# Kernel optimization log

Hardware: AMD Instinct MI355X
Metric: run time of the kernel (lower is better)

The kernel has to match this reference:

```python
import jax, jax.numpy as jnp
import numpy as np

IN_FEATURES = 512
HIDDEN = 512


def setup_inputs() -> dict:
    key = jax.random.key(0)
    ks = jax.random.split(key, 7)
    s = 1.0 / np.sqrt(IN_FEATURES)
    return {
        "x": jax.random.normal(ks[0], (8, 2048, IN_FEATURES), dtype=jnp.float32),
        "Wq": jax.random.uniform(ks[1], (IN_FEATURES, HIDDEN), jnp.float32, -s, s),
        "bq": jax.random.uniform(ks[2], (HIDDEN,), jnp.float32, -s, s),
        "Wk": jax.random.uniform(ks[3], (IN_FEATURES, HIDDEN), jnp.float32, -s, s),
        "bk": jax.random.uniform(ks[4], (HIDDEN,), jnp.float32, -s, s),
        "Wv": jax.random.uniform(ks[5], (IN_FEATURES, HIDDEN), jnp.float32, -s, s),
        "bv": jax.random.uniform(ks[6], (HIDDEN,), jnp.float32, -s, s),
    }


def reference(x, Wq, bq, Wk, bk, Wv, bv):
    # q,k,v: [b, s, h]
    q = jnp.einsum("bsf,fh->bsh", x, Wq) + bq
    k = jnp.einsum("bsf,fh->bsh", x, Wk) + bk
    v = jnp.einsum("bsf,fh->bsh", x, Wv) + bv
    # NOTE: no 1/sqrt(d) scaling, matching the original module.
    scores = jnp.einsum("bqh,bkh->bqk", q, k)  # [b, s, s]
    attn = jax.nn.softmax(scores, axis=-1)
    return jnp.einsum("bqk,bkh->bqh", attn, v)
```

## Files before the change

### kernel.cpp

```cpp
#include <hip/hip_runtime.h>
#include <hip/hip_fp16.h>


typedef _Float16 f16;
typedef __attribute__((ext_vector_type(8))) _Float16 f16x8;
typedef __attribute__((ext_vector_type(4))) _Float16 f16x4;
typedef __attribute__((ext_vector_type(4))) float f32x4;
typedef __attribute__((address_space(3))) char lds_t;

#define GADDR(p) ((const __attribute__((address_space(1))) void*)(p))
#define LADDR(p) ((__attribute__((address_space(3))) void*)(p))

__device__ __forceinline__ unsigned lds_u32(void* p) {
    return (unsigned)(unsigned long long)(lds_t*)p;
}

#define DSRD(dst, a) asm volatile("ds_read_b128 %0, %1" : "=v"(dst) : "v"(a))
#define WAITV0 asm volatile("s_waitcnt vmcnt(0)" ::: "memory")
#define WAITV4 asm volatile("s_waitcnt vmcnt(4)" ::: "memory")
#define WAITV8 asm volatile("s_waitcnt vmcnt(8)" ::: "memory")
#define WAITLGKM0 asm volatile("s_waitcnt lgkmcnt(0)" ::: "memory")

__device__ __forceinline__ void xcd_remap(int& bx, int& by, int& bz) {
    const int gx = gridDim.x, gy = gridDim.y;
    const int nwg = gx * gy * gridDim.z;
    const int f = (blockIdx.z * gy + blockIdx.y) * gx + blockIdx.x;
    int L = (f & 7) * (nwg >> 3) + (f >> 3);
    bx = L % gx; int r = L / gx; by = r % gy; bz = r / gy;
}

__global__ __launch_bounds__(256) void k_cvt_x(const float* __restrict__ in,
                                               f16* __restrict__ out) {
    long i = (long)blockIdx.x * 256 + threadIdx.x;
    float4 v = ((const float4*)in)[i];
    f16x4 h = { (f16)v.x, (f16)v.y, (f16)v.z, (f16)v.w };
    ((f16x4*)out)[i] = h;
}

__global__ __launch_bounds__(256) void k_cvt_w(const float* __restrict__ Wq,
                                               const float* __restrict__ Wk,
                                               const float* __restrict__ Wv,
                                               f16* __restrict__ Wt) {
    int id = blockIdx.x * 256 + threadIdx.x;
    int w = id >> 18, rem = id & 262143;
    int kk = rem >> 9, n = rem & 511;
    const float* W = (w == 0) ? Wq : (w == 1) ? Wk : Wv;
    Wt[((long)w << 18) + ((long)n << 9) + kk] = (f16)W[((long)kk << 9) + n];
}

__global__ __launch_bounds__(256) void k_transpose_v(const f16* __restrict__ V,
                                                     f16* __restrict__ Vt) {
    __shared__ f16 t[32][33];
    int b = blockIdx.z, s0 = blockIdx.y * 32, d0 = blockIdx.x * 32;
    int x = threadIdx.x & 31, y = threadIdx.x >> 5;
#pragma unroll
    for (int i = 0; i < 4; ++i)
        t[y + i * 8][x] = V[((long)(b * 2048 + s0 + y + i * 8) << 9) + d0 + x];
    __syncthreads();
#pragma unroll
    for (int i = 0; i < 4; ++i)
        Vt[((long)(b * 512 + d0 + y + i * 8) << 11) + s0 + x] = t[x][y + i * 8];
}


#define STAGE8(HBASE, SRC, LD, ROWB, K0)                                                        \
  { const f16* s0_ = (SRC) + ((ROWB) + (tid >> 3)) * (long)(LD) + (K0) + colSw;                 \
    __builtin_amdgcn_global_load_lds(GADDR(s0_), LADDR(smem + (HBASE) + wid * 1024), 16, 0, 0); \
    const f16* s1_ = (SRC) + ((ROWB) + 64 + (tid >> 3)) * (long)(LD) + (K0) + colSw;            \
    __builtin_amdgcn_global_load_lds(GADDR(s1_), LADDR(smem + (HBASE) + 8192 + wid * 1024), 16, 0, 0); }

#define PHASE8(BUF, MH, NH, STAGE_CODE, WAIT_CODE)                                   \
  {                                                                                  \
    f16x8 af[4][2], bf[2][2];                                                        \
    const unsigned aB = sbase + (BUF) * 65536u + (MH) * 16384u;                      \
    const unsigned bB = sbase + (BUF) * 65536u + 32768u + (NH) * 16384u;             \
    _Pragma("unroll") for (int mi = 0; mi < 4; ++mi) {                               \
      unsigned ra = wm2 * 64 + mi * 16 + l15;                                        \
      DSRD(af[mi][0], aB + ra * 128 + cb0);                                          \
      DSRD(af[mi][1], aB + ra * 128 + cb1);                                          \
    }                                                                                \
    _Pragma("unroll") for (int nj = 0; nj < 2; ++nj) {                               \
      unsigned rb = wn2 * 32 + nj * 16 + l15;                                        \
      DSRD(bf[nj][0], bB + rb * 128 + cb0);                                          \
      DSRD(bf[nj][1], bB + rb * 128 + cb1);                                          \
    }                                                                                \
    STAGE_CODE;                                                                      \
    WAIT_CODE;                                                                       \
    __builtin_amdgcn_s_barrier();                                                    \
    WAITLGKM0;                                                                       \
    __builtin_amdgcn_sched_barrier(0);                                               \
    __builtin_amdgcn_s_setprio(1);                                                   \
    _Pragma("unroll") for (int mi = 0; mi < 4; ++mi)                                 \
      _Pragma("unroll") for (int nj = 0; nj < 2; ++nj)                               \
        _Pragma("unroll") for (int ks = 0; ks < 2; ++ks)                             \
          acc[MH][NH][mi][nj] = __builtin_amdgcn_mfma_f32_16x16x32_f16(              \
              af[mi][ks], bf[nj][ks], acc[MH][NH][mi][nj], 0, 0, 0);                 \
    __builtin_amdgcn_s_setprio(0);                                                   \
    __builtin_amdgcn_s_barrier();                                                    \
  }

template <bool OUT_F16, bool QKV>
__global__ __launch_bounds__(512) void k_gemm8(const f16* __restrict__ A,
                                               const f16* __restrict__ Bt,
                                               void* __restrict__ Cv,
                                               void* __restrict__ CvAlt,
                                               const float* __restrict__ b0,
                                               const float* __restrict__ b1,
                                               const float* __restrict__ b2,
                                               int M, int N, int K,
                                               long sA, long sB, long sC) {
    int bxi, byi, bz;
    xcd_remap(bxi, byi, bz);
    A  += bz * sA;
    Bt += bz * sB;
    __shared__ __align__(16) char smem[131072];
    const unsigned sbase = lds_u32(smem);

    const int tid = threadIdx.x;
    const int wid = tid >> 6, lane = tid & 63;
    const int l15 = lane & 15, l4 = lane >> 4;
    const int wm2 = wid >> 2, wn2 = wid & 3;
    const long rowA0 = (long)byi * 256;
    const long rowB0 = (long)bxi * 256;

    const unsigned sw = (unsigned)((l15 & 7) << 4);
    const unsigned cb0 = (unsigned)(l4 * 16) ^ sw;
    const unsigned cb1 = (unsigned)(64 + l4 * 16) ^ sw;
    const int colSw = (((tid & 7) ^ ((tid >> 3) & 7)) << 3);

    f32x4 acc[2][2][4][2] = {};

    const int NT = K >> 6;

    STAGE8(0,             A,  K, rowA0,       0);
    STAGE8(32768,         Bt, K, rowB0,       0);
    STAGE8(16384,         A,  K, rowA0 + 128, 0);
    STAGE8(32768 + 16384, Bt, K, rowB0 + 128, 0);
    STAGE8(65536,         A,  K, rowA0,       64);
    STAGE8(65536 + 32768, Bt, K, rowB0,       64);
    WAITV4;
    __builtin_amdgcn_s_barrier();

    for (int t = 0; t < NT; t += 2) {
        const bool more = (t + 2 < NT);
        const int k1 = (t + 1) << 6, k2 = (t + 2) << 6, k3 = (t + 3) << 6;
        PHASE8(0, 0, 0, { STAGE8(65536 + 16384,         A,  K, rowA0 + 128, k1); }, );
        PHASE8(0, 0, 1, { STAGE8(65536 + 32768 + 16384, Bt, K, rowB0 + 128, k1); }, );
        PHASE8(0, 1, 0, { if (more) STAGE8(0,             A,  K, rowA0,       k2); }, );
        PHASE8(0, 1, 1, { if (more) STAGE8(32768,         Bt, K, rowB0,       k2); },
                        { if (more) WAITV4; else WAITV0; });
        PHASE8(1, 0, 0, { if (more) STAGE8(16384,         A,  K, rowA0 + 128, k2); }, );
        PHASE8(1, 0, 1, { if (more) STAGE8(32768 + 16384, Bt, K, rowB0 + 128, k2); }, );
        PHASE8(1, 1, 0, { if (more) STAGE8(65536,         A,  K, rowA0,       k3); }, );
        PHASE8(1, 1, 1, { if (more) STAGE8(65536 + 32768, Bt, K, rowB0,       k3); },
                        { if (more) WAITV4; else WAITV0; });
    }

    const float* bias = nullptr;
    if constexpr (QKV) bias = (bz == 0) ? b0 : (bz == 1) ? b1 : b2;

#pragma unroll
    for (int MH = 0; MH < 2; ++MH)
#pragma unroll
        for (int NH = 0; NH < 2; ++NH)
#pragma unroll
            for (int mi = 0; mi < 4; ++mi)
#pragma unroll
                for (int nj = 0; nj < 2; ++nj) {
                    long gr = rowA0 + MH * 128 + wm2 * 64 + mi * 16 + l4 * 4;
                    int  gc = (int)rowB0 + NH * 128 + wn2 * 32 + nj * 16 + l15;
                    float bv_ = QKV ? bias[gc] : 0.f;
                    if constexpr (OUT_F16) {
                        f16* C;
                        if constexpr (QKV) C = (bz < 2) ? (f16*)Cv + bz * sC : (f16*)CvAlt;
                        else               C = (f16*)Cv + bz * sC;
#pragma unroll
                        for (int r = 0; r < 4; ++r)
                            C[(gr + r) * (long)N + gc] = (f16)(acc[MH][NH][mi][nj][r] + bv_);
                    } else {
                        float* C = (float*)Cv + bz * sC;
#pragma unroll
                        for (int r = 0; r < 4; ++r)
                            C[(gr + r) * (long)N + gc] = acc[MH][NH][mi][nj][r] + bv_;
                    }
                }
}

#define PVSTAGE(BUF, K0)                                                                    \
  { _Pragma("unroll") for (int i_ = 0; i_ < 4; ++i_) {                                      \
      const f16* sa_ = A + (rowA0 + i_ * 32 + (tid >> 3)) * (long)K + (K0) + colSw;         \
      __builtin_amdgcn_global_load_lds(GADDR(sa_),                                          \
          LADDR(smem + (BUF) * 32768 + i_ * 4096 + wave * 1024), 16, 0, 0);                 \
      const f16* sb_ = Bt + (rowB0 + i_ * 32 + (tid >> 3)) * (long)K + (K0) + colSw;        \
      __builtin_amdgcn_global_load_lds(GADDR(sb_),                                          \
          LADDR(smem + (BUF) * 32768 + 16384 + i_ * 4096 + wave * 1024), 16, 0, 0);         \
    } }

__global__ __launch_bounds__(256) void k_pv(const f16* __restrict__ Ain,
                                            const f16* __restrict__ Btin,
                                            float* __restrict__ Cout,
                                            int N, int K,
                                            long sA, long sB, long sC) {
    int bxi, byi, bz;
    xcd_remap(bxi, byi, bz);
    const f16* A  = Ain  + bz * sA;
    const f16* Bt = Btin + bz * sB;
    __shared__ __align__(16) char smem[65536];
    const unsigned sbase = lds_u32(smem);

    const int tid = threadIdx.x;
    const int wave = tid >> 6, lane = tid & 63;
    const int l15 = lane & 15, l4 = lane >> 4;
    const int wm = (wave >> 1) * 64, wn = (wave & 1) * 64;
    const long rowA0 = (long)byi * 128;
    const long rowB0 = (long)bxi * 128;

    const unsigned sw = (unsigned)((l15 & 7) << 4);
    const unsigned cb0 = (unsigned)(l4 * 16) ^ sw;
    const unsigned cb1 = (unsigned)(64 + l4 * 16) ^ sw;
    const int colSw = (((tid & 7) ^ ((tid >> 3) & 7)) << 3);

    f32x4 acc[4][4] = {};

    const int nt = K >> 6;
    PVSTAGE(0, 0);
    int cur = 0;
    for (int t = 0; t < nt; ++t) {
        if (t + 1 < nt) { PVSTAGE(cur ^ 1, (t + 1) << 6); WAITV8; }
        else            { WAITV0; }
        __builtin_amdgcn_s_barrier();

        f16x8 af[4][2], bf[4][2];
        const unsigned aB = sbase + (unsigned)cur * 32768u;
        const unsigned bB = aB + 16384u;
#pragma unroll
        for (int mi = 0; mi < 4; ++mi) {
            unsigned ra = wm + mi * 16 + l15;
            DSRD(af[mi][0], aB + ra * 128 + cb0);
            DSRD(af[mi][1], aB + ra * 128 + cb1);
        }
#pragma unroll
        for (int nj = 0; nj < 4; ++nj) {
            unsigned rb = wn + nj * 16 + l15;
            DSRD(bf[nj][0], bB + rb * 128 + cb0);
            DSRD(bf[nj][1], bB + rb * 128 + cb1);
        }
        WAITLGKM0;
        __builtin_amdgcn_sched_barrier(0);
        __builtin_amdgcn_s_setprio(1);
#pragma unroll
        for (int mi = 0; mi < 4; ++mi)
#pragma unroll
            for (int nj = 0; nj < 4; ++nj)
#pragma unroll
                for (int ks = 0; ks < 2; ++ks)
                    acc[mi][nj] = __builtin_amdgcn_mfma_f32_16x16x32_f16(
                        af[mi][ks], bf[nj][ks], acc[mi][nj], 0, 0, 0);
        __builtin_amdgcn_s_setprio(0);
        __builtin_amdgcn_s_barrier();
        cur ^= 1;
    }

    float* C = Cout + bz * sC;
#pragma unroll
    for (int mi = 0; mi < 4; ++mi)
#pragma unroll
        for (int nj = 0; nj < 4; ++nj) {
            long gr = rowA0 + wm + mi * 16 + l4 * 4;
            int  gc = (int)rowB0 + wn + nj * 16 + l15;
#pragma unroll
            for (int r = 0; r < 4; ++r)
                C[(gr + r) * (long)N + gc] = acc[mi][nj][r];
        }
}

__global__ __launch_bounds__(256) void k_softmax(f16* __restrict__ P) {
    const long row = blockIdx.x;
    f16* p = P + row * 2048;
    const int tid = threadIdx.x, lane = tid & 63, wave = tid >> 6;

    f16x8 v = ((const f16x8*)p)[tid];
    float f[8];
#pragma unroll
    for (int j = 0; j < 8; ++j) f[j] = (float)v[j];
    float m = fmaxf(fmaxf(fmaxf(f[0], f[1]), fmaxf(f[2], f[3])),
                    fmaxf(fmaxf(f[4], f[5]), fmaxf(f[6], f[7])));
#pragma unroll
    for (int off = 32; off; off >>= 1) m = fmaxf(m, __shfl_xor(m, off));

    __shared__ float red[4];
    __shared__ float bc[2];
    if (lane == 0) red[wave] = m;
    __syncthreads();
    if (tid == 0) bc[0] = fmaxf(fmaxf(red[0], red[1]), fmaxf(red[2], red[3]));
    __syncthreads();
    m = bc[0];

    float e[8], sum = 0.f;
#pragma unroll
    for (int j = 0; j < 8; ++j) { e[j] = __expf(f[j] - m); sum += e[j]; }
#pragma unroll
    for (int off = 32; off; off >>= 1) sum += __shfl_xor(sum, off);
    if (lane == 0) red[wave] = sum;
    __syncthreads();
    if (tid == 0) bc[1] = (red[0] + red[1]) + (red[2] + red[3]);
    __syncthreads();
    float inv = 1.f / bc[1];

    f16x8 o;
#pragma unroll
    for (int j = 0; j < 8; ++j) o[j] = (f16)(e[j] * inv);
    ((f16x8*)p)[tid] = o;
}

extern "C" void kernel_launch(void* const* d_in, const int* in_sizes, int n_in,
                              void* d_out, int out_size, void* d_ws, size_t ws_size,
                              hipStream_t stream) {
    const float* x  = (const float*)d_in[0];
    const float* Wq = (const float*)d_in[1];
    const float* bq = (const float*)d_in[2];
    const float* Wk = (const float*)d_in[3];
    const float* bk = (const float*)d_in[4];
    const float* Wv = (const float*)d_in[5];
    const float* bv = (const float*)d_in[6];
    float* out = (float*)d_out;

    char* ws = (char*)d_ws;
    f16* qh = (f16*)(ws + 0);
    f16* kh = (f16*)(ws + 16777216);
    f16* P8 = (f16*)(ws + 33554432);
    f16* Wt = (f16*)(ws + 33554432);
    f16* vt = (f16*)(ws + 0);
    f16* xh = (f16*)d_out;
    f16* vv = (f16*)((char*)d_out + 16777216);

    k_cvt_x<<<8192, 256, 0, stream>>>(x, xh);
    k_cvt_w<<<3072, 256, 0, stream>>>(Wq, Wk, Wv, Wt);

    k_gemm8<true, true><<<dim3(2, 64, 3), 512, 0, stream>>>(
        xh, Wt, qh, vv, bq, bk, bv, 16384, 512, 512,
        0, (long)512 * 512, (long)16384 * 512);

    k_gemm8<true, false><<<dim3(8, 8, 8), 512, 0, stream>>>(
        qh, kh, P8, nullptr, nullptr, nullptr, nullptr, 2048, 2048, 512,
        (long)2048 * 512, (long)2048 * 512, (long)2048 * 2048);

    k_transpose_v<<<dim3(16, 64, 8), 256, 0, stream>>>(vv, vt);

    k_softmax<<<16384, 256, 0, stream>>>(P8);

    k_pv<<<dim3(4, 16, 8), 256, 0, stream>>>(
        P8, vt, out, 512, 2048,
        (long)2048 * 2048, (long)512 * 2048, (long)2048 * 512);
}
```

Measured before the change: 174.4 us.

## Software-pipeline LDS fragment loads across MFMA phases with double-buffered A fragments

Restructures the GEMM inner loop from eight phases of 16 MFMAs into four phases of 32 MFMAs. B fragments for both N halves load once per K-tile, and A fragments are double-buffered in registers so the next phase's LDS reads run during the current phase's MFMAs. Partial lgkmcnt waits replace full drains, and the number of barriers per K-tile pair drops. This adds register pressure from the extra fragment sets and relies on careful ordering of the LDS waits.

New measurement: 299.2 us. 1.72x slower.

```diff
diff --git a/kernel.cpp b/kernel.cpp
--- a/kernel.cpp
+++ b/kernel.cpp
@@ -19,7 +19,7 @@
 #define WAITV0 asm volatile("s_waitcnt vmcnt(0)" ::: "memory")
 #define WAITV4 asm volatile("s_waitcnt vmcnt(4)" ::: "memory")
 #define WAITV8 asm volatile("s_waitcnt vmcnt(8)" ::: "memory")
-#define WAITLGKM0 asm volatile("s_waitcnt lgkmcnt(0)" ::: "memory")
+#define WAITLG(n) asm volatile("s_waitcnt lgkmcnt(" #n ")" ::: "memory")
 
 __device__ __forceinline__ void xcd_remap(int& bx, int& by, int& bz) {
     const int gx = gridDim.x, gy = gridDim.y;
@@ -69,35 +69,32 @@
     const f16* s1_ = (SRC) + ((ROWB) + 64 + (tid >> 3)) * (long)(LD) + (K0) + colSw;            \
     __builtin_amdgcn_global_load_lds(GADDR(s1_), LADDR(smem + (HBASE) + 8192 + wid * 1024), 16, 0, 0); }
 
-#define PHASE8(BUF, MH, NH, STAGE_CODE, WAIT_CODE)                                   \
-  {                                                                                  \
-    f16x8 af[4][2], bf[2][2];                                                        \
-    const unsigned aB = sbase + (BUF) * 65536u + (MH) * 16384u;                      \
-    const unsigned bB = sbase + (BUF) * 65536u + 32768u + (NH) * 16384u;             \
-    _Pragma("unroll") for (int mi = 0; mi < 4; ++mi) {                               \
-      unsigned ra = wm2 * 64 + mi * 16 + l15;                                        \
-      DSRD(af[mi][0], aB + ra * 128 + cb0);                                          \
-      DSRD(af[mi][1], aB + ra * 128 + cb1);                                          \
-    }                                                                                \
+#define LOAD_AF(AFSET, BUF, MH)                                                      \
+  _Pragma("unroll") for (int mi = 0; mi < 4; ++mi) {                                 \
+    unsigned ra = wm2 * 64 + mi * 16 + l15;                                          \
+    DSRD(AFSET[mi][0], sbase + (BUF) * 65536u + (MH) * 16384u + ra * 128 + cb0);     \
+    DSRD(AFSET[mi][1], sbase + (BUF) * 65536u + (MH) * 16384u + ra * 128 + cb1);     \
+  }
+
+#define LOAD_BF(BUF)                                                                 \
+  _Pragma("unroll") for (int nh = 0; nh < 2; ++nh)                                   \
     _Pragma("unroll") for (int nj = 0; nj < 2; ++nj) {                               \
       unsigned rb = wn2 * 32 + nj * 16 + l15;                                        \
-      DSRD(bf[nj][0], bB + rb * 128 + cb0);                                          \
-      DSRD(bf[nj][1], bB + rb * 128 + cb1);                                          \
-    }                                                                                \
-    STAGE_CODE;                                                                      \
-    WAIT_CODE;                                                                       \
-    __builtin_amdgcn_s_barrier();                                                    \
-    WAITLGKM0;                                                                       \
-    __builtin_amdgcn_sched_barrier(0);                                               \
-    __builtin_amdgcn_s_setprio(1);                                                   \
-    _Pragma("unroll") for (int mi = 0; mi < 4; ++mi)                                 \
+      DSRD(bf[nh][nj][0], sbase + (BUF) * 65536u + 32768u + nh * 16384u + rb * 128 + cb0); \
+      DSRD(bf[nh][nj][1], sbase + (BUF) * 65536u + 32768u + nh * 16384u + rb * 128 + cb1); \
+    }
+
+#define MFMA_Q(MH, AFSET)                                                            \
+  __builtin_amdgcn_sched_barrier(0);                                                 \
+  __builtin_amdgcn_s_setprio(1);                                                     \
+  _Pragma("unroll") for (int mi = 0; mi < 4; ++mi)                                   \
+    _Pragma("unroll") for (int nh = 0; nh < 2; ++nh)                                 \
       _Pragma("unroll") for (int nj = 0; nj < 2; ++nj)                               \
         _Pragma("unroll") for (int ks = 0; ks < 2; ++ks)                             \
-          acc[MH][NH][mi][nj] = __builtin_amdgcn_mfma_f32_16x16x32_f16(              \
-              af[mi][ks], bf[nj][ks], acc[MH][NH][mi][nj], 0, 0, 0);                 \
-    __builtin_amdgcn_s_setprio(0);                                                   \
-    __builtin_amdgcn_s_barrier();                                                    \
-  }
+          acc[MH][nh][mi][nj] = __builtin_amdgcn_mfma_f32_16x16x32_f16(              \
+              AFSET[mi][ks], bf[nh][nj][ks], acc[MH][nh][mi][nj], 0, 0, 0);          \
+  __builtin_amdgcn_s_setprio(0);                                                     \
+  __builtin_amdgcn_s_barrier();
 
 template <bool OUT_F16, bool QKV>
 __global__ __launch_bounds__(512) void k_gemm8(const f16* __restrict__ A,
@@ -128,6 +125,7 @@
     const unsigned cb1 = (unsigned)(64 + l4 * 16) ^ sw;
     const int colSw = (((tid & 7) ^ ((tid >> 3) & 7)) << 3);
 
+    f16x8 afA[4][2], afB[4][2], bf[2][2][2];
     f32x4 acc[2][2][4][2] = {};
 
     const int NT = K >> 6;
@@ -140,20 +138,46 @@
     STAGE8(65536 + 32768, Bt, K, rowB0,       64);
     WAITV4;
     __builtin_amdgcn_s_barrier();
+    LOAD_AF(afA, 0, 0);
 
     for (int t = 0; t < NT; t += 2) {
         const bool more = (t + 2 < NT);
         const int k1 = (t + 1) << 6, k2 = (t + 2) << 6, k3 = (t + 3) << 6;
-        PHASE8(0, 0, 0, { STAGE8(65536 + 16384,         A,  K, rowA0 + 128, k1); }, );
-        PHASE8(0, 0, 1, { STAGE8(65536 + 32768 + 16384, Bt, K, rowB0 + 128, k1); }, );
-        PHASE8(0, 1, 0, { if (more) STAGE8(0,             A,  K, rowA0,       k2); }, );
-        PHASE8(0, 1, 1, { if (more) STAGE8(32768,         Bt, K, rowB0,       k2); },
-                        { if (more) WAITV4; else WAITV0; });
-        PHASE8(1, 0, 0, { if (more) STAGE8(16384,         A,  K, rowA0 + 128, k2); }, );
-        PHASE8(1, 0, 1, { if (more) STAGE8(32768 + 16384, Bt, K, rowB0 + 128, k2); }, );
-        PHASE8(1, 1, 0, { if (more) STAGE8(65536,         A,  K, rowA0,       k3); }, );
-        PHASE8(1, 1, 1, { if (more) STAGE8(65536 + 32768, Bt, K, rowB0,       k3); },
-                        { if (more) WAITV4; else WAITV0; });
+
+        STAGE8(65536 + 16384,         A,  K, rowA0 + 128, k1);
+        STAGE8(65536 + 32768 + 16384, Bt, K, rowB0 + 128, k1);
+        __builtin_amdgcn_s_barrier();
+        LOAD_BF(0);
+        LOAD_AF(afB, 0, 1);
+        WAITLG(8);
+        MFMA_Q(0, afA);
+
+        if (more) { STAGE8(0,     A,  K, rowA0, k2);
+                    STAGE8(32768, Bt, K, rowB0, k2);
+                    WAITV4; }
+        else      { WAITV0; }
+        __builtin_amdgcn_s_barrier();
+        LOAD_AF(afA, 1, 0);
+        WAITLG(8);
+        MFMA_Q(1, afB);
+
+        if (more) { STAGE8(16384,         A,  K, rowA0 + 128, k2);
+                    STAGE8(32768 + 16384, Bt, K, rowB0 + 128, k2); }
+        __builtin_amdgcn_s_barrier();
+        LOAD_BF(1);
+        LOAD_AF(afB, 1, 1);
+        WAITLG(8);
+        MFMA_Q(0, afA);
+
+        if (more) { STAGE8(65536,         A,  K, rowA0, k3);
+                    STAGE8(65536 + 32768, Bt, K, rowB0, k3);
+                    WAITV4; }
+        else      { WAITV0; }
+        __builtin_amdgcn_s_barrier();
+        if (more) { LOAD_AF(afA, 0, 0);
+                    WAITLG(8); }
+        else      { WAITLG(0); }
+        MFMA_Q(1, afB);
     }
 
     const float* bias = nullptr;
@@ -245,7 +269,7 @@
             DSRD(bf[nj][0], bB + rb * 128 + cb0);
             DSRD(bf[nj][1], bB + rb * 128 + cb1);
         }
-        WAITLGKM0;
+        WAITLG(0);
         __builtin_amdgcn_sched_barrier(0);
         __builtin_amdgcn_s_setprio(1);
 #pragma unroll
```
